# Optimization experiments

Hardware: AMD Instinct MI355X
Metric: run time of the kernel (lower is better)

Reference implementation:

```python
import jax, jax.numpy as jnp
import numpy as np

R = 2           # local_radius
N_HEADS = 4     # num_heads
OUT = 256       # out_channels


def _attn_scale(x, Wq, bq, Wk, bk, Wv, bv):
    # Faithful jax port of SparseSelfAttention.forward
    B, C, H, W = x.shape
    N = H * W
    d = OUT // N_HEADS
    # torch x.view(B, N, -1) on contiguous [B,C,H,W] == row-major reshape
    xf = x.reshape(B, N, C)
    q = (xf @ Wq.T + bq).reshape(B, N, N_HEADS, d).transpose(0, 2, 1, 3)  # [B,h,N,d]
    k = (xf @ Wk.T + bk).reshape(B, N, N_HEADS, d).transpose(0, 2, 1, 3)
    v = (xf @ Wv.T + bv).reshape(B, N, N_HEADS, d).transpose(0, 2, 1, 3)
    scale = 1.0 / np.sqrt(OUT).astype(np.float32)
    acc = jnp.zeros_like(v)
    for dh in range(-R, R + 1):
        for dw in range(-R, R + 1):
            # original rolls dims (-3,-2) of [B,h,N,d] -> (head, point) dims
            rk = jnp.roll(k, (dh, dw), axis=(1, 2))
            s = jnp.einsum('bhnd,bhmd->bhnm', q, rk) * scale  # [B,h,N,N]
            a = jax.nn.softmax(s, axis=-1)                     # dropout p=0.0
            rv = jnp.roll(v, (-dh, -dw), axis=(1, 2))
            acc = acc + jnp.einsum('bhnm,bhmd->bhnd', a, rv)
    return acc.transpose(0, 2, 1, 3).reshape(B, N, OUT)  # [B,N,out]


def setup_inputs() -> dict:
    key = jax.random.key(0)
    ks = jax.random.split(key, 8)
    B, C, H, W = 2, 256, 32, 32
    std = 1.0 / np.sqrt(C)
    d = {
        'x0': jax.random.normal(ks[0], (B, C, H, W), jnp.float32),
        'x1': jax.random.normal(ks[1], (B, C, H, W), jnp.float32),
    }
    i = 2
    for s in (0, 1):
        for p in ('q', 'k', 'v'):
            d[f'W{p}{s}'] = jax.random.uniform(ks[i], (OUT, C), jnp.float32, -std, std)
            d[f'b{p}{s}'] = jnp.zeros((OUT,), jnp.float32)
            i += 1
    return d


def reference(x0, x1, Wq0, bq0, Wk0, bk0, Wv0, bv0,
              Wq1, bq1, Wk1, bk1, Wv1, bv1):
    out0 = _attn_scale(x0, Wq0, bq0, Wk0, bk0, Wv0, bv0)
    out1 = _attn_scale(x1, Wq1, bq1, Wk1, bk1, Wv1, bv1)
    return out0 + out1  # [B, N, out_channels], summed across scales
```

## Files before the change

### kernel.cpp

```cpp
#include <hip/hip_runtime.h>
#include <hip/hip_bf16.h>


typedef __bf16 bf16x8 __attribute__((ext_vector_type(8)));
typedef __bf16 bf16x4 __attribute__((ext_vector_type(4)));
typedef float f32x4 __attribute__((ext_vector_type(4)));

#define MFMA16(A,B,C) __builtin_amdgcn_mfma_f32_16x16x32_bf16(A,B,C,0,0,0)

__device__ __forceinline__ bf16x8 ld8(const __bf16* p){ return *reinterpret_cast<const bf16x8*>(p); }

struct ProjArgs { const float* W[6]; const float* Bz[6]; };

__global__ __launch_bounds__(256) void cvt_k(const float* __restrict__ x0,
                                             const float* __restrict__ x1,
                                             ProjArgs args,
                                             __bf16* __restrict__ Xb,
                                             __bf16* __restrict__ Wb)
{
    int g = blockIdx.x*256 + threadIdx.x;
    const float* src; __bf16* dst;
    if (g < 131072){
        int s = g >> 16;
        int E = (g & 65535)*8;
        int blk = E >> 9, lane8 = (E >> 3) & 63;
        int row = (blk>>3)*16 + (lane8 & 15);
        int ci  = (blk&7)*32 + (lane8>>4)*8;
        src = (s ? x1 : x0) + (size_t)row*256 + ci;
        dst = Xb + (size_t)s*524288 + E;
    } else {
        int gw = g - 131072;
        int sp = gw >> 13;
        int E = (gw & 8191)*8;
        int blk = E >> 9, lane8 = (E >> 3) & 63;
        int co = (blk>>3)*16 + (lane8 & 15);
        int ci = (blk&7)*32 + (lane8>>4)*8;
        src = args.W[sp] + (size_t)co*256 + ci;
        dst = Wb + (size_t)sp*65536 + E;
    }
    f32x4 a = *reinterpret_cast<const f32x4*>(src);
    f32x4 b = *reinterpret_cast<const f32x4*>(src+4);
    bf16x8 o;
    #pragma unroll
    for (int j=0;j<4;j++){ o[j] = (__bf16)a[j]; o[4+j] = (__bf16)b[j]; }
    *reinterpret_cast<bf16x8*>(dst) = o;
}

__global__ __launch_bounds__(256) void proj_k(const __bf16* __restrict__ Xb,
                                              const __bf16* __restrict__ Wb,
                                              ProjArgs args,
                                              __bf16* __restrict__ Qb,
                                              __bf16* __restrict__ Kb,
                                              __bf16* __restrict__ Vb)
{
    __shared__ __bf16 stage[4096];
    int bid = blockIdx.x;
    int cg = bid % 12, rg = bid / 12;
    int tid = threadIdx.x, wv = tid >> 6, l = tid & 63;
    int lr = l & 15, lg = l >> 4;
    int s = rg >> 5;
    const __bf16* Xf = Xb + (size_t)s*524288;
    int p = cg >> 2;
    const __bf16* Wf = Wb + (size_t)(s*3+p)*65536;
    const float* bp = args.Bz[s*3 + p];
    int colbase = (cg & 3)*64;
    int rowblk = ((rg & 31)*4 + wv);

    f32x4 acc[4];
    #pragma unroll
    for (int t=0;t<4;t++) acc[t] = f32x4{0.f,0.f,0.f,0.f};

    #pragma unroll
    for (int kk=0; kk<8; kk++){
        bf16x8 af = ld8(Xf + (size_t)(rowblk*8 + kk)*512 + l*8);
        #pragma unroll
        for (int ct=0; ct<4; ct++){
            bf16x8 bfv = ld8(Wf + (size_t)(((cg&3)*4 + ct)*8 + kk)*512 + l*8);
            acc[ct] = MFMA16(af, bfv, acc[ct]);
        }
    }
    float qs = (p==0) ? 0.09016844136f : 1.0f;
    #pragma unroll
    for (int ct=0; ct<4; ct++){
        int d = ct*16 + lr;
        float bias = bp[colbase + d];
        #pragma unroll
        for (int i=0;i<4;i++){
            float v = (acc[ct][i] + bias) * qs;
            int a;
            if (p < 2) a = wv*1024 + ((d>>5)&1)*512 + ((d>>3)&3)*128 + (lg*4+i)*8 + (d&7);
            else       a = (wv*16 + lg*4 + i)*64 + d;
            stage[a] = (__bf16)v;
        }
    }
    __syncthreads();
    int gr0 = rg*64;
    int b = (gr0 >> 10) & 1, n0 = gr0 & 1023;
    int h = cg & 3;
    int sb = s*2 + b;
    __bf16* dstb; size_t goff;
    if (p == 0){ dstb = Qb; goff = ((size_t)(sb*4 + h))*65536 + (size_t)(n0>>4)*1024; }
    else if (p == 1){ dstb = Kb; goff = ((size_t)(sb*4 + h))*65536 + (size_t)(n0>>4)*1024; }
    else { dstb = Vb; goff = ((size_t)(sb*4 + h)*1024 + n0)*64; }
    bf16x8 v0 = *reinterpret_cast<const bf16x8*>(stage + tid*16);
    bf16x8 v1 = *reinterpret_cast<const bf16x8*>(stage + tid*16 + 8);
    *reinterpret_cast<bf16x8*>(dstb + goff + (size_t)tid*16)     = v0;
    *reinterpret_cast<bf16x8*>(dstb + goff + (size_t)tid*16 + 8) = v1;
}

__global__ __launch_bounds__(256) void smooth_k(const __bf16* __restrict__ Vb,
                                                __bf16* __restrict__ WT)
{
    __shared__ __bf16 Vt[72][66];
    int bid = blockIdx.x;
    int sbu = bid >> 4, n0 = (bid & 15)*64;
    int tid = threadIdx.x;
    const __bf16* Vs = Vb + (size_t)sbu*65536;
    for (int idx = tid; idx < 576; idx += 256){
        int row = idx >> 3, ch = idx & 7;
        int n = (n0 - 4 + row) & 1023;
        bf16x8 v = ld8(Vs + (size_t)n*64 + ch*8);
        #pragma unroll
        for (int j=0;j<8;j++) Vt[row][ch*8+j] = v[j];
    }
    __syncthreads();
    int w = tid >> 6, l = tid & 63;
    __bf16* dst = WT + (size_t)sbu*65536;
    int m = n0 + l;
    int kb = m >> 5, m32 = m & 31;
    int p = (m32 < 16) ? ((m32>>2)*8 + (m32&3))
                       : (((m32-16)>>2)*8 + 4 + (m32&3));
    size_t pbase = (size_t)kb*2048 + (p>>3)*128 + (p&7);
    #pragma unroll
    for (int it=0; it<16; it++){
        int d = it*4 + w;
        float sum = 0.f;
        #pragma unroll
        for (int j=0;j<5;j++) sum += (float)Vt[l + j*2][d];
        dst[pbase + (size_t)(d>>4)*512 + (d&15)*8] = (__bf16)sum;
    }
}

__global__ __launch_bounds__(256) void attn_k(const __bf16* __restrict__ Qb,
                                              const __bf16* __restrict__ Kb,
                                              const __bf16* __restrict__ WT,
                                              __bf16* __restrict__ pvp,
                                              float* __restrict__ dsp)
{
    int tid = threadIdx.x, wv = tid>>6, l = tid&63, lr = l&15, lg = l>>4;
    int t = blockIdx.x;
    int qg = t & 7; t >>= 3;
    int dhi = t & 3, h = (t>>2)&3, b = (t>>4)&1, s = (t>>5)&1;
    int dhv = (dhi==2) ? -1 : (dhi==3 ? 2 : dhi);
    int g = (h - dhv + 4) & 3;
    int u = (h + dhv + 4) & 3;
    int sb = s*2 + b;
    int nbase = qg*128 + wv*32;
    const __bf16* Qw = Qb + ((size_t)(sb*4 + h))*65536 + (size_t)(nbase>>4)*1024;
    const __bf16* Kg = Kb + ((size_t)(sb*4 + g))*65536;
    const __bf16* Wu = WT + ((size_t)(sb*4 + u))*65536;
    bf16x8 qa0 = ld8(Qw + l*8),        qa1 = ld8(Qw + 512 + l*8);
    bf16x8 qb0 = ld8(Qw + 1024 + l*8), qb1 = ld8(Qw + 1536 + l*8);

    const f32x4 z = {0.f,0.f,0.f,0.f};
    f32x4 pvA[4] = {z,z,z,z};
    f32x4 pvB[4] = {z,z,z,z};
    float dsA = 0.f, dsB = 0.f;

    for (int kt=0; kt<1024; kt+=32){
        const __bf16* k0 = Kg + (size_t)(kt>>4)*1024 + l*8;
        bf16x8 kf00 = ld8(k0),        kf01 = ld8(k0 + 512);
        bf16x8 kf10 = ld8(k0 + 1024), kf11 = ld8(k0 + 1536);
        const __bf16* w0 = Wu + (size_t)(kt>>5)*2048 + l*8;
        bf16x8 wd0 = ld8(w0);
        bf16x8 wd1 = ld8(w0 + 512);
        bf16x8 wd2 = ld8(w0 + 1024);
        bf16x8 wd3 = ld8(w0 + 1536);
        f32x4 sA0 = MFMA16(kf00, qa0, z); sA0 = MFMA16(kf01, qa1, sA0);
        f32x4 sA1 = MFMA16(kf10, qa0, z); sA1 = MFMA16(kf11, qa1, sA1);
        f32x4 sB0 = MFMA16(kf00, qb0, z); sB0 = MFMA16(kf01, qb1, sB0);
        f32x4 sB1 = MFMA16(kf10, qb0, z); sB1 = MFMA16(kf11, qb1, sB1);
        bf16x8 paA, paB;
        #pragma unroll
        for (int i=0;i<4;i++){
            float eA0 = __builtin_amdgcn_exp2f(sA0[i]);
            float eA1 = __builtin_amdgcn_exp2f(sA1[i]);
            float eB0 = __builtin_amdgcn_exp2f(sB0[i]);
            float eB1 = __builtin_amdgcn_exp2f(sB1[i]);
            dsA += eA0 + eA1;
            dsB += eB0 + eB1;
            paA[i] = (__bf16)eA0; paA[4+i] = (__bf16)eA1;
            paB[i] = (__bf16)eB0; paB[4+i] = (__bf16)eB1;
        }
        pvA[0] = MFMA16(wd0, paA, pvA[0]);
        pvA[1] = MFMA16(wd1, paA, pvA[1]);
        pvA[2] = MFMA16(wd2, paA, pvA[2]);
        pvA[3] = MFMA16(wd3, paA, pvA[3]);
        pvB[0] = MFMA16(wd0, paB, pvB[0]);
        pvB[1] = MFMA16(wd1, paB, pvB[1]);
        pvB[2] = MFMA16(wd2, paB, pvB[2]);
        pvB[3] = MFMA16(wd3, paB, pvB[3]);
    }
    dsA += __shfl_xor(dsA, 16, 64); dsA += __shfl_xor(dsA, 32, 64);
    dsB += __shfl_xor(dsB, 16, 64); dsB += __shfl_xor(dsB, 32, 64);

    int slot = s*4 + dhi;
    __bf16* pp = pvp + (size_t)slot*524288;
    #pragma unroll
    for (int dt=0; dt<4; dt++){
        bf16x4 oA, oB;
        #pragma unroll
        for (int i=0;i<4;i++){ oA[i] = (__bf16)pvA[dt][i]; oB[i] = (__bf16)pvB[dt][i]; }
        size_t col = (size_t)h*64 + dt*16 + lg*4;
        *reinterpret_cast<bf16x4*>(pp + ((size_t)b*1024 + nbase + lr)*256 + col)      = oA;
        *reinterpret_cast<bf16x4*>(pp + ((size_t)b*1024 + nbase + 16 + lr)*256 + col) = oB;
    }
    if (l < 16){
        dsp[(size_t)slot*8192 + ((size_t)b*4+h)*1024 + nbase + l]      = dsA;
        dsp[(size_t)slot*8192 + ((size_t)b*4+h)*1024 + nbase + 16 + l] = dsB;
    }
}

__global__ __launch_bounds__(256) void reduce_k(const __bf16* __restrict__ pvp,
                                                const float* __restrict__ dsp,
                                                float* __restrict__ out)
{
    int idx = blockIdx.x*256 + threadIdx.x;
    int c8 = idx & 31, bn = idx >> 5;
    int h = c8 >> 3;
    size_t dsoff = (size_t)(bn>>10)*4096 + (size_t)h*1024 + (bn & 1023);
    float acc[8] = {0,0,0,0,0,0,0,0};
    #pragma unroll
    for (int s4=0; s4<8; s4++){
        float wgt = ((s4&3)==3) ? 2.f : 1.f;
        bf16x8 v = ld8(pvp + (size_t)s4*524288 + (size_t)bn*256 + c8*8);
        float DS = dsp[(size_t)s4*8192 + dsoff];
        float sc = wgt / DS;
        #pragma unroll
        for (int j=0;j<8;j++) acc[j] += (float)v[j] * sc;
    }
    f32x4 o0 = {acc[0],acc[1],acc[2],acc[3]};
    f32x4 o1 = {acc[4],acc[5],acc[6],acc[7]};
    *reinterpret_cast<f32x4*>(out + (size_t)idx*8)     = o0;
    *reinterpret_cast<f32x4*>(out + (size_t)idx*8 + 4) = o1;
}

extern "C" void kernel_launch(void* const* d_in, const int* in_sizes, int n_in,
                              void* d_out, int out_size, void* d_ws, size_t ws_size,
                              hipStream_t stream)
{
    const float* x0 = (const float*)d_in[0];
    const float* x1 = (const float*)d_in[1];
    ProjArgs pa;
    for (int s=0;s<2;s++) for (int p=0;p<3;p++){
        pa.W[s*3+p]  = (const float*)d_in[2 + s*6 + p*2];
        pa.Bz[s*3+p] = (const float*)d_in[3 + s*6 + p*2];
    }
    char* wsb = (char*)d_ws;
    __bf16* Qb = (__bf16*)(wsb);
    __bf16* Kb = (__bf16*)(wsb + (2u<<20));
    __bf16* Vb = (__bf16*)(wsb + (4u<<20));
    __bf16* WT = (__bf16*)(wsb + (6u<<20));
    __bf16* Xb = (__bf16*)(wsb + (8u<<20));
    __bf16* Wb = (__bf16*)(wsb + (10u<<20));
    __bf16* pvp = (__bf16*)(wsb + (11u<<20));
    float*  dsp = (float*)(wsb + (19u<<20));

    cvt_k<<<704, 256, 0, stream>>>(x0, x1, pa, Xb, Wb);
    proj_k<<<768, 256, 0, stream>>>(Xb, Wb, pa, Qb, Kb, Vb);
    smooth_k<<<256, 256, 0, stream>>>(Vb, WT);
    attn_k<<<512, 256, 0, stream>>>(Qb, Kb, WT, pvp, dsp);
    reduce_k<<<256, 256, 0, stream>>>(pvp, dsp, (float*)d_out);
}
```

Measured before the change: 51.73 us.

## Normalize softmax in attention epilogue, stage stores via LDS, add MFMA priority hints

```diff
diff --git a/kernel.cpp b/kernel.cpp
--- a/kernel.cpp
+++ b/kernel.cpp
@@ -144,8 +144,7 @@
 __global__ __launch_bounds__(256) void attn_k(const __bf16* __restrict__ Qb,
                                               const __bf16* __restrict__ Kb,
                                               const __bf16* __restrict__ WT,
-                                              __bf16* __restrict__ pvp,
-                                              float* __restrict__ dsp)
+                                              __bf16* __restrict__ pvp)
 {
     int tid = threadIdx.x, wv = tid>>6, l = tid&63, lr = l&15, lg = l>>4;
     int t = blockIdx.x;
@@ -167,6 +166,7 @@
     f32x4 pvB[4] = {z,z,z,z};
     float dsA = 0.f, dsB = 0.f;
 
+    #pragma unroll 2
     for (int kt=0; kt<1024; kt+=32){
         const __bf16* k0 = Kg + (size_t)(kt>>4)*1024 + l*8;
         bf16x8 kf00 = ld8(k0),        kf01 = ld8(k0 + 512);
@@ -176,10 +176,12 @@
         bf16x8 wd1 = ld8(w0 + 512);
         bf16x8 wd2 = ld8(w0 + 1024);
         bf16x8 wd3 = ld8(w0 + 1536);
+        __builtin_amdgcn_s_setprio(1);
         f32x4 sA0 = MFMA16(kf00, qa0, z); sA0 = MFMA16(kf01, qa1, sA0);
         f32x4 sA1 = MFMA16(kf10, qa0, z); sA1 = MFMA16(kf11, qa1, sA1);
         f32x4 sB0 = MFMA16(kf00, qb0, z); sB0 = MFMA16(kf01, qb1, sB0);
         f32x4 sB1 = MFMA16(kf10, qb0, z); sB1 = MFMA16(kf11, qb1, sB1);
+        __builtin_amdgcn_s_setprio(0);
         bf16x8 paA, paB;
         #pragma unroll
         for (int i=0;i<4;i++){
@@ -192,6 +194,7 @@
             paA[i] = (__bf16)eA0; paA[4+i] = (__bf16)eA1;
             paB[i] = (__bf16)eB0; paB[4+i] = (__bf16)eB1;
         }
+        __builtin_amdgcn_s_setprio(1);
         pvA[0] = MFMA16(wd0, paA, pvA[0]);
         pvA[1] = MFMA16(wd1, paA, pvA[1]);
         pvA[2] = MFMA16(wd2, paA, pvA[2]);
@@ -200,49 +203,50 @@
         pvB[1] = MFMA16(wd1, paB, pvB[1]);
         pvB[2] = MFMA16(wd2, paB, pvB[2]);
         pvB[3] = MFMA16(wd3, paB, pvB[3]);
+        __builtin_amdgcn_s_setprio(0);
     }
     dsA += __shfl_xor(dsA, 16, 64); dsA += __shfl_xor(dsA, 32, 64);
     dsB += __shfl_xor(dsB, 16, 64); dsB += __shfl_xor(dsB, 32, 64);
-
-    int slot = s*4 + dhi;
-    __bf16* pp = pvp + (size_t)slot*524288;
+    float wgt = (dhi==3) ? 2.f : 1.f;
+    float invA = wgt / dsA, invB = wgt / dsB;
+
+    __shared__ alignas(16) __bf16 ost[4][32*72];
+    __bf16* S = ost[wv];
     #pragma unroll
     for (int dt=0; dt<4; dt++){
         bf16x4 oA, oB;
         #pragma unroll
-        for (int i=0;i<4;i++){ oA[i] = (__bf16)pvA[dt][i]; oB[i] = (__bf16)pvB[dt][i]; }
-        size_t col = (size_t)h*64 + dt*16 + lg*4;
-        *reinterpret_cast<bf16x4*>(pp + ((size_t)b*1024 + nbase + lr)*256 + col)      = oA;
-        *reinterpret_cast<bf16x4*>(pp + ((size_t)b*1024 + nbase + 16 + lr)*256 + col) = oB;
-    }
-    if (l < 16){
-        dsp[(size_t)slot*8192 + ((size_t)b*4+h)*1024 + nbase + l]      = dsA;
-        dsp[(size_t)slot*8192 + ((size_t)b*4+h)*1024 + nbase + 16 + l] = dsB;
+        for (int i=0;i<4;i++){ oA[i] = (__bf16)(pvA[dt][i]*invA); oB[i] = (__bf16)(pvB[dt][i]*invB); }
+        int c0 = dt*16 + lg*4;
+        *reinterpret_cast<bf16x4*>(S + lr*72 + c0)      = oA;
+        *reinterpret_cast<bf16x4*>(S + (16+lr)*72 + c0) = oB;
+    }
+    int slot = s*4 + dhi;
+    __bf16* pp = pvp + (size_t)slot*524288 + (size_t)b*262144 + (size_t)h*64;
+    #pragma unroll
+    for (int it=0; it<4; it++){
+        int r = it*8 + (l>>3);
+        bf16x8 v = *reinterpret_cast<const bf16x8*>(S + r*72 + (l&7)*8);
+        *reinterpret_cast<bf16x8*>(pp + (size_t)(nbase + r)*256 + (l&7)*8) = v;
     }
 }
 
 __global__ __launch_bounds__(256) void reduce_k(const __bf16* __restrict__ pvp,
-                                                const float* __restrict__ dsp,
                                                 float* __restrict__ out)
 {
     int idx = blockIdx.x*256 + threadIdx.x;
-    int c8 = idx & 31, bn = idx >> 5;
-    int h = c8 >> 3;
-    size_t dsoff = (size_t)(bn>>10)*4096 + (size_t)h*1024 + (bn & 1023);
+    size_t off = (size_t)idx*8;
     float acc[8] = {0,0,0,0,0,0,0,0};
     #pragma unroll
     for (int s4=0; s4<8; s4++){
-        float wgt = ((s4&3)==3) ? 2.f : 1.f;
-        bf16x8 v = ld8(pvp + (size_t)s4*524288 + (size_t)bn*256 + c8*8);
-        float DS = dsp[(size_t)s4*8192 + dsoff];
-        float sc = wgt / DS;
-        #pragma unroll
-        for (int j=0;j<8;j++) acc[j] += (float)v[j] * sc;
+        bf16x8 v = ld8(pvp + (size_t)s4*524288 + off);
+        #pragma unroll
+        for (int j=0;j<8;j++) acc[j] += (float)v[j];
     }
     f32x4 o0 = {acc[0],acc[1],acc[2],acc[3]};
     f32x4 o1 = {acc[4],acc[5],acc[6],acc[7]};
-    *reinterpret_cast<f32x4*>(out + (size_t)idx*8)     = o0;
-    *reinterpret_cast<f32x4*>(out + (size_t)idx*8 + 4) = o1;
+    *reinterpret_cast<f32x4*>(out + off)     = o0;
+    *reinterpret_cast<f32x4*>(out + off + 4) = o1;
 }
 
 extern "C" void kernel_launch(void* const* d_in, const int* in_sizes, int n_in,
@@ -264,11 +268,10 @@
     __bf16* Xb = (__bf16*)(wsb + (8u<<20));
     __bf16* Wb = (__bf16*)(wsb + (10u<<20));
     __bf16* pvp = (__bf16*)(wsb + (11u<<20));
-    float*  dsp = (float*)(wsb + (19u<<20));
 
     cvt_k<<<704, 256, 0, stream>>>(x0, x1, pa, Xb, Wb);
     proj_k<<<768, 256, 0, stream>>>(Xb, Wb, pa, Qb, Kb, Vb);
     smooth_k<<<256, 256, 0, stream>>>(Vb, WT);
-    attn_k<<<512, 256, 0, stream>>>(Qb, Kb, WT, pvp, dsp);
-    reduce_k<<<256, 256, 0, stream>>>(pvp, dsp, (float*)d_out);
-}
+    attn_k<<<512, 256, 0, stream>>>(Qb, Kb, WT, pvp);
+    reduce_k<<<256, 256, 0, stream>>>(pvp, (float*)d_out);
+}
```

Result: faster. 47.88 us (-7.4%).
